# Performance work log

Measured on AMD Instinct MI355X. Metric: run time of the kernel, lower is better.

## Reference

```python
import jax, jax.numpy as jnp
import numpy as np

N_NODES = 100000
N_EDGES = 400000
HIDDEN = 256
N_LAYERS = 4
HEADS = 8
MAX_DEPTH = 20
NUM_GRAPHS = 128
SEQ_LEN = 5
VOCAB = 5002  # vocab_size + 2
NEG_SLOPE = 0.2
BN_EPS = 1e-5


def setup_inputs() -> dict:
    key = jax.random.key(0)
    ks = jax.random.split(key, 16)
    x = jax.random.randint(ks[0], (N_NODES, 2), 0, 98, dtype=jnp.int32)
    node_depth = jax.random.randint(ks[1], (N_NODES, 1), 0, MAX_DEPTH + 1, dtype=jnp.int32)
    edge_index = jax.random.randint(ks[2], (2, N_EDGES), 0, N_NODES, dtype=jnp.int32)
    batch = jnp.sort(jax.random.randint(ks[3], (N_NODES,), 0, NUM_GRAPHS, dtype=jnp.int32))
    s = 1.0 / np.sqrt(HIDDEN)
    return {
        "x": x,
        "node_depth": node_depth,
        "edge_index": edge_index,
        "batch": batch,
        "type_emb": jax.random.normal(ks[4], (98, HIDDEN), jnp.float32) * s,
        "attr_emb": jax.random.normal(ks[5], (10030, HIDDEN), jnp.float32) * s,
        "depth_emb": jax.random.normal(ks[6], (MAX_DEPTH + 1, HIDDEN), jnp.float32) * s,
        "Ws": jax.random.normal(ks[7], (N_LAYERS, HIDDEN, HIDDEN), jnp.float32) * s,
        "att_src": jax.random.normal(ks[8], (N_LAYERS, HIDDEN), jnp.float32) * s,
        "att_dst": jax.random.normal(ks[9], (N_LAYERS, HIDDEN), jnp.float32) * s,
        "gat_bias": jnp.zeros((N_LAYERS, HIDDEN), jnp.float32),
        "bn_gamma": jnp.ones((N_LAYERS, HIDDEN), jnp.float32),
        "bn_beta": jnp.zeros((N_LAYERS, HIDDEN), jnp.float32),
        "tok_W": jax.random.normal(ks[10], (SEQ_LEN, HIDDEN, VOCAB), jnp.float32) * s,
        "tok_b": jnp.zeros((SEQ_LEN, VOCAB), jnp.float32),
    }


def _gat_layer(h, src, dst, W, a_src, a_dst, bias, heads):
    # h: [N, HIDDEN]; PyG GATConv v1 with concat heads, self-loops already in (src, dst)
    N = h.shape[0]
    d = HIDDEN // heads
    hh = (h @ W).reshape(N, heads, d)                       # [N, H, d]
    s_src = jnp.einsum("nhd,hd->nh", hh, a_src.reshape(heads, d))
    s_dst = jnp.einsum("nhd,hd->nh", hh, a_dst.reshape(heads, d))
    e = jax.nn.leaky_relu(s_src[src] + s_dst[dst], NEG_SLOPE)  # [E, H]
    m = jax.ops.segment_max(e, dst, num_segments=N)           # [N, H]
    ex = jnp.exp(e - m[dst])
    denom = jax.ops.segment_sum(ex, dst, num_segments=N)      # [N, H]
    alpha = ex / denom[dst]                                    # [E, H]
    msg = hh[src] * alpha[:, :, None]                          # [E, H, d]
    out = jax.ops.segment_sum(msg, dst, num_segments=N)       # [N, H, d]
    return out.reshape(N, HIDDEN) + bias


def _batchnorm(h, gamma, beta):
    mu = jnp.mean(h, axis=0)
    var = jnp.var(h, axis=0)
    return (h - mu) * jax.lax.rsqrt(var + BN_EPS) * gamma + beta


def reference(x, node_depth, edge_index, batch, type_emb, attr_emb, depth_emb,
              Ws, att_src, att_dst, gat_bias, bn_gamma, bn_beta, tok_W, tok_b):
    N = x.shape[0]
    depth = jnp.minimum(node_depth.reshape(-1), MAX_DEPTH)
    h = type_emb[x[:, 0]] + attr_emb[x[:, 1]] + depth_emb[depth]  # [N, HIDDEN]

    # add self loops (PyG GATConv default)
    loop = jnp.arange(N, dtype=edge_index.dtype)
    src = jnp.concatenate([edge_index[0], loop])
    dst = jnp.concatenate([edge_index[1], loop])

    heads_per_layer = [HEADS] * (N_LAYERS - 1) + [1]
    for l in range(N_LAYERS):
        identity = h
        h = _gat_layer(h, src, dst, Ws[l], att_src[l], att_dst[l], gat_bias[l], heads_per_layer[l])
        h = _batchnorm(h, bn_gamma[l], bn_beta[l])
        h = jax.nn.relu(h)
        h = h + identity  # residual

    # mean pool per graph
    counts = jax.ops.segment_sum(jnp.ones((N,), h.dtype), batch, num_segments=NUM_GRAPHS)
    g = jax.ops.segment_sum(h, batch, num_segments=NUM_GRAPHS) / jnp.maximum(counts, 1.0)[:, None]

    # seq_len token predictors -> [SEQ_LEN, G, VOCAB]
    preds = jnp.einsum("gh,shv->sgv", g, tok_W) + tok_b[:, None, :]
    return preds
```

## Files before the change

kernel.cpp:

```cpp
#include <hip/hip_runtime.h>
#include <stdint.h>

typedef uint16_t u16;
typedef uint32_t u32;

#define N_NODESC 100000
#define N_EDGESC 400000
#define E_TOT    500000
#define HID      256
#define NLAYERS  4
#define NGRAPHS  128
#define SEQLEN   5
#define VOCABC   5002
#define MAXDEPTH 20
#define NEG_SLOPE 0.2f
#define BN_EPSC  1e-5f
#define NCHUNK   ((N_NODESC + 255)/256)
#define NCH64    ((N_NODESC + 63)/64)
#define NROWT    (N_NODESC/16)
#define NPART    64
#define NVQ      ((VOCABC + 63)/64)
#define ATTNB    2048
#define LDSROW   264

typedef __attribute__((ext_vector_type(8))) short short8;
typedef __attribute__((ext_vector_type(4))) float f32x4;
typedef __attribute__((ext_vector_type(4))) unsigned short u16x4;

__device__ __forceinline__ float b2f(u16 u){
  union { u32 i; float f; } v; v.i = ((u32)u) << 16; return v.f;
}
__device__ __forceinline__ u16 f2b(float f){
  union { float f; u32 i; } v; v.f = f;
  u32 u = v.i;
  u += 0x7FFFu + ((u >> 16) & 1u);
  return (u16)(u >> 16);
}
__device__ __forceinline__ float ldp(const void* p, size_t i, int f){
  return f ? ((const float*)p)[i] : b2f(((const u16*)p)[i]);
}
__device__ __forceinline__ f32x4 ld4(const void* p, size_t i, int f){
  f32x4 r;
  if (f){
    r = *(const f32x4*)((const float*)p + i);
  } else {
    const u16x4 u = *(const u16x4*)((const u16*)p + i);
    r[0] = b2f(u[0]); r[1] = b2f(u[1]); r[2] = b2f(u[2]); r[3] = b2f(u[3]);
  }
  return r;
}

__global__ __launch_bounds__(64) void k_detect(const void* temb, int* flag){
  int lane = threadIdx.x;
  const u32* w32 = (const u32*)temb;
  int sf = 0, sb = 0;
  for (int i = lane; i < 256; i += 64){
    u32 w = w32[i];
    union { u32 u; float f; } cf; cf.u = w;
    float af = fabsf(cf.f);
    if (cf.f == 0.0f || (af >= 1e-12f && af <= 4096.f)) sf++;
    float b0 = b2f((u16)(w & 0xFFFFu));
    float b1 = b2f((u16)(w >> 16));
    float a0 = fabsf(b0), a1 = fabsf(b1);
    if (b0 == 0.f || (a0 >= 1e-12f && a0 <= 4096.f)) sb++;
    if (b1 == 0.f || (a1 >= 1e-12f && a1 <= 4096.f)) sb++;
  }
  #pragma unroll
  for (int o = 1; o < 64; o <<= 1){ sf += __shfl_xor(sf, o); sb += __shfl_xor(sb, o); }
  if (lane == 0) *flag = (2*sf > sb) ? 1 : 0;
}

__global__ __launch_bounds__(256) void k_zero(int* __restrict__ p, int n){
  int i = blockIdx.x*256 + threadIdx.x;
  if (i < n) p[i] = 0;
}

__global__ __launch_bounds__(256) void k_embed(const int* __restrict__ x, const int* __restrict__ nd,
    const void* __restrict__ temb, const void* __restrict__ aemb, const void* __restrict__ demb,
    u16* __restrict__ h, const int* __restrict__ flagp, int* __restrict__ cursor){
  int f = *flagp;
  int tid = threadIdx.x;
  int r0 = blockIdx.x*64;
  if (tid < 64 && r0 + tid < N_NODESC) cursor[r0 + tid] = 0;
  int wid = tid >> 6, lane = tid & 63;
  int c4 = lane*4;
  #pragma unroll 4
  for (int k = 0; k < 16; ++k){
    int n = r0 + wid*16 + k;
    if (n >= N_NODESC) break;
    int t = x[n*2+0], a = x[n*2+1];
    if (t < 0) t = 0; if (t > 97) t = 97;
    if (a < 0) a = 0; if (a > 10029) a = 10029;
    int d = nd[n]; if (d > MAXDEPTH) d = MAXDEPTH; if (d < 0) d = 0;
    const f32x4 vt = ld4(temb, (size_t)t*HID + c4, f);
    const f32x4 va = ld4(aemb, (size_t)a*HID + c4, f);
    const f32x4 vd = ld4(demb, (size_t)d*HID + c4, f);
    u16x4 o;
    #pragma unroll
    for (int j = 0; j < 4; ++j) o[j] = f2b(vt[j] + va[j] + vd[j]);
    *(u16x4*)(h + (size_t)n*HID + c4) = o;
  }
}

__global__ __launch_bounds__(256) void k_hist(const int* __restrict__ ei, int* __restrict__ cnt){
  int e = blockIdx.x*256 + threadIdx.x;
  if (e >= E_TOT) return;
  int dst = (e < N_EDGESC) ? ei[N_EDGESC + e] : (e - N_EDGESC);
  if ((unsigned)dst >= N_NODESC) return;
  atomicAdd(&cnt[dst], 1);
}

__global__ __launch_bounds__(256) void k_scan_part(const int* __restrict__ cnt,
    int* __restrict__ off, int* __restrict__ btot){
  __shared__ int lds[256];
  int b = blockIdx.x, tid = threadIdx.x;
  int i = b*256 + tid;
  int v = (i < N_NODESC) ? cnt[i] : 0;
  lds[tid] = v;
  __syncthreads();
  #pragma unroll
  for (int s = 1; s < 256; s <<= 1){
    int t = (tid >= s) ? lds[tid - s] : 0;
    __syncthreads();
    lds[tid] += t;
    __syncthreads();
  }
  if (i < N_NODESC) off[i] = lds[tid] - v;
  if (tid == 255) btot[b] = lds[255];
}

__global__ __launch_bounds__(256) void k_scan_tot(const int* __restrict__ btot,
    int* __restrict__ boff, int* __restrict__ offN){
  __shared__ int lds[256];
  __shared__ int s_carry;
  int tid = threadIdx.x;
  if (tid == 0) s_carry = 0;
  __syncthreads();
  for (int base = 0; base < NCHUNK; base += 256){
    int i = base + tid;
    int v = (i < NCHUNK) ? btot[i] : 0;
    lds[tid] = v;
    __syncthreads();
    #pragma unroll
    for (int s = 1; s < 256; s <<= 1){
      int t = (tid >= s) ? lds[tid - s] : 0;
      __syncthreads();
      lds[tid] += t;
      __syncthreads();
    }
    if (i < NCHUNK) boff[i] = s_carry + lds[tid] - v;
    __syncthreads();
    if (tid == 255) s_carry += lds[255];
    __syncthreads();
  }
  if (tid == 0) *offN = s_carry;
}

__global__ __launch_bounds__(256) void k_scan_add(int* __restrict__ off,
    const int* __restrict__ boff, int* __restrict__ cursor){
  int b = blockIdx.x;
  int i = b*256 + threadIdx.x;
  if (i < N_NODESC){ off[i] += boff[b]; cursor[i] = 0; }
}

__global__ __launch_bounds__(256) void k_scatter(const int* __restrict__ ei,
    const int* __restrict__ soff, int* __restrict__ cursor, int* __restrict__ ssorted){
  int e = blockIdx.x*256 + threadIdx.x;
  if (e >= E_TOT) return;
  int src = (e < N_EDGESC) ? ei[e]            : (e - N_EDGESC);
  int dst = (e < N_EDGESC) ? ei[N_EDGESC + e] : (e - N_EDGESC);
  if ((unsigned)dst >= N_NODESC || (unsigned)src >= N_NODESC) return;
  int pos = soff[dst] + atomicAdd(&cursor[dst], 1);
  if ((unsigned)pos < E_TOT) ssorted[pos] = src;
}

__global__ __launch_bounds__(256) void k_transW(const void* __restrict__ W, u16* __restrict__ WT,
    const int* __restrict__ flagp){
  int f = *flagp;
  int l = blockIdx.y, n2 = blockIdx.x, k = threadIdx.x;
  WT[(l*HID + n2)*HID + k] = f2b(ldp(W, (size_t)(l*HID + k)*HID + n2, f));
}

__global__ __launch_bounds__(256) void k_prepVA(const void* __restrict__ Ws,
    const void* __restrict__ asrc, const void* __restrict__ adst,
    u16* __restrict__ VAT, const int* __restrict__ flagp){
  int f = *flagp;
  int l = blockIdx.x;
  int i = threadIdx.x;
  int H = (l == NLAYERS-1) ? 1 : 8;
  float col[16];
  #pragma unroll
  for (int c = 0; c < 16; ++c) col[c] = 0.f;
  if (H == 8){
    for (int h = 0; h < 8; ++h){
      float vs = 0.f, vd = 0.f;
      for (int o = h*32; o < h*32+32; ++o){
        float w = ldp(Ws, ((size_t)l*HID + i)*HID + o, f);
        vs += w * ldp(asrc, (size_t)l*HID + o, f);
        vd += w * ldp(adst, (size_t)l*HID + o, f);
      }
      col[h*2] = vs; col[h*2+1] = vd;
    }
  } else {
    float vs = 0.f, vd = 0.f;
    for (int o = 0; o < HID; ++o){
      float w = ldp(Ws, ((size_t)l*HID + i)*HID + o, f);
      vs += w * ldp(asrc, (size_t)l*HID + o, f);
      vd += w * ldp(adst, (size_t)l*HID + o, f);
    }
    col[0] = vs; col[1] = vd;
  }
  #pragma unroll
  for (int c = 0; c < 16; ++c)
    VAT[((size_t)l*16 + c)*HID + i] = f2b(col[c]);
}

__global__ __launch_bounds__(256) void k_gemm(u16* __restrict__ h,
    const u16* __restrict__ gout, const float* __restrict__ scale,
    const float* __restrict__ shift, int doApply,
    const u16* __restrict__ WT, const u16* __restrict__ VAT,
    u16* __restrict__ hh, float* __restrict__ ssrc, float* __restrict__ sdst,
    int H, float* __restrict__ bnpart){
  __shared__ u16 hA[2][16*LDSROW];
  int tid = threadIdx.x;
  if (blockIdx.x < NPART*2) bnpart[blockIdx.x*256 + tid] = 0.f;
  int wave = tid >> 6, lane = tid & 63;
  int m = lane & 15, quad = lane >> 4;
  int prow = tid >> 4, pch = (tid & 15)*16;

  short8 B[4][8];
  #pragma unroll
  for (int j = 0; j < 4; ++j){
    const u16* wp = WT + (size_t)((wave*4 + j)*16 + m)*HID + quad*8;
    #pragma unroll
    for (int ks = 0; ks < 8; ++ks)
      B[j][ks] = *(const short8*)(wp + ks*32);
  }
  short8 B5[8];
  if (wave == 0){
    const u16* vp = VAT + (size_t)m*HID + quad*8;
    #pragma unroll
    for (int ks = 0; ks < 8; ++ks)
      B5[ks] = *(const short8*)(vp + ks*32);
  }

  f32x4 sc0 = {}, sc1 = {}, sc2 = {}, sc3 = {};
  f32x4 sh0 = {}, sh1 = {}, sh2 = {}, sh3 = {};
  if (doApply){
    sc0 = *(const f32x4*)(scale + pch);      sh0 = *(const f32x4*)(shift + pch);
    sc1 = *(const f32x4*)(scale + pch + 4);  sh1 = *(const f32x4*)(shift + pch + 4);
    sc2 = *(const f32x4*)(scale + pch + 8);  sh2 = *(const f32x4*)(shift + pch + 8);
    sc3 = *(const f32x4*)(scale + pch + 12); sh3 = *(const f32x4*)(shift + pch + 12);
  }

  int t = blockIdx.x;
  if (t >= NROWT) return;

  short8 h0, h1, g0 = {}, g1 = {};
  {
    size_t base = (size_t)(t*16 + prow)*HID + pch;
    h0 = *(const short8*)(h + base);
    h1 = *(const short8*)(h + base + 8);
    if (doApply){
      g0 = *(const short8*)(gout + base);
      g1 = *(const short8*)(gout + base + 8);
    }
  }

  int p = 0;
  for (;;){
    {
      size_t base = (size_t)(t*16 + prow)*HID + pch;
      if (doApply){
        #pragma unroll
        for (int j = 0; j < 4; ++j){
          float tv = b2f((u16)g0[j])*sc0[j] + sh0[j];
          tv = (tv > 0.f) ? tv : 0.f;
          h0[j] = (short)f2b(b2f((u16)h0[j]) + tv);
        }
        #pragma unroll
        for (int j = 0; j < 4; ++j){
          float tv = b2f((u16)g0[4+j])*sc1[j] + sh1[j];
          tv = (tv > 0.f) ? tv : 0.f;
          h0[4+j] = (short)f2b(b2f((u16)h0[4+j]) + tv);
        }
        #pragma unroll
        for (int j = 0; j < 4; ++j){
          float tv = b2f((u16)g1[j])*sc2[j] + sh2[j];
          tv = (tv > 0.f) ? tv : 0.f;
          h1[j] = (short)f2b(b2f((u16)h1[j]) + tv);
        }
        #pragma unroll
        for (int j = 0; j < 4; ++j){
          float tv = b2f((u16)g1[4+j])*sc3[j] + sh3[j];
          tv = (tv > 0.f) ? tv : 0.f;
          h1[4+j] = (short)f2b(b2f((u16)h1[4+j]) + tv);
        }
        *(short8*)(h + base)     = h0;
        *(short8*)(h + base + 8) = h1;
      }
      *(short8*)(&hA[p][prow*LDSROW + pch])     = h0;
      *(short8*)(&hA[p][prow*LDSROW + pch + 8]) = h1;
    }

    int tn = t + gridDim.x;
    bool hn = (tn < NROWT);
    short8 nh0 = h0, nh1 = h1, ng0 = g0, ng1 = g1;
    if (hn){
      size_t nbase = (size_t)(tn*16 + prow)*HID + pch;
      nh0 = *(const short8*)(h + nbase);
      nh1 = *(const short8*)(h + nbase + 8);
      if (doApply){
        ng0 = *(const short8*)(gout + nbase);
        ng1 = *(const short8*)(gout + nbase + 8);
      }
    }

    asm volatile("s_waitcnt lgkmcnt(0)" ::: "memory");
    __builtin_amdgcn_s_barrier();

    short8 A[8];
    #pragma unroll
    for (int ks = 0; ks < 8; ++ks)
      A[ks] = *(const short8*)(&hA[p][m*LDSROW + ks*32 + quad*8]);

    f32x4 acc[4];
    #pragma unroll
    for (int j = 0; j < 4; ++j) acc[j] = (f32x4){0.f,0.f,0.f,0.f};
    #pragma unroll
    for (int ks = 0; ks < 8; ++ks){
      #pragma unroll
      for (int j = 0; j < 4; ++j)
        acc[j] = __builtin_amdgcn_mfma_f32_16x16x32_bf16(A[ks], B[j][ks], acc[j], 0, 0, 0);
    }

    int r0 = t*16;
    if (wave == 0){
      f32x4 acc5 = (f32x4){0.f,0.f,0.f,0.f};
      #pragma unroll
      for (int ks = 0; ks < 8; ++ks)
        acc5 = __builtin_amdgcn_mfma_f32_16x16x32_bf16(A[ks], B5[ks], acc5, 0, 0, 0);
      int hidx = m >> 1, sd = m & 1;
      #pragma unroll
      for (int r = 0; r < 4; ++r){
        int row = r0 + quad*4 + r;
        float val = acc5[r];
        if (H == 8){
          if (sd == 0) ssrc[row*8 + hidx] = val;
          else         sdst[row*8 + hidx] = val;
        } else {
          if (m == 0)      ssrc[row] = val;
          else if (m == 1) sdst[row] = val;
        }
      }
    }

    #pragma unroll
    for (int j = 0; j < 4; ++j){
      int col = (wave*4 + j)*16 + m;
      #pragma unroll
      for (int r = 0; r < 4; ++r){
        int orow = r0 + quad*4 + r;
        hh[(size_t)orow*HID + col] = f2b(acc[j][r]);
      }
    }

    if (!hn) break;
    t = tn; p ^= 1;
    h0 = nh0; h1 = nh1; g0 = ng0; g1 = ng1;
  }
}

__device__ __forceinline__ void attn_node(int n, int lane, const u16* __restrict__ hh,
    const float* __restrict__ ssrc, const float* __restrict__ sdst,
    const int* __restrict__ soff, const int* __restrict__ ssorted, int H, float r[4]){
  int f0 = lane*4;
  int hl = (H == 8) ? (lane >> 3) : 0;
  float sd = sdst[n*H + hl];
  int beg = soff[n], end = soff[n+1];
  if (beg < 0) beg = 0;
  if (end > E_TOT) end = E_TOT;
  r[0] = r[1] = r[2] = r[3] = 0.f;
  if (beg >= end) return;
  int src = ssorted[beg];
  if ((unsigned)src >= N_NODESC) src = n;
  u16x4 hvv = *(const u16x4*)(hh + (size_t)src*HID + f0);
  float es = ssrc[src*H + hl];
  float lval = 0.f;
  float o0 = 0.f, o1 = 0.f, o2 = 0.f, o3 = 0.f;
  for (int i = beg; i < end; ++i){
    int nsrc = src;
    if (i + 1 < end){
      nsrc = ssorted[i+1];
      if ((unsigned)nsrc >= N_NODESC) nsrc = src;
    }
    const u16x4 nh = *(const u16x4*)(hh + (size_t)nsrc*HID + f0);
    const float nes = ssrc[nsrc*H + hl];
    float ev = es + sd;
    ev = (ev > 0.f) ? ev : NEG_SLOPE*ev;
    ev = fminf(fmaxf(ev, -60.f), 60.f);
    float wv = __expf(ev);
    lval += wv;
    o0 += wv*b2f(hvv[0]);
    o1 += wv*b2f(hvv[1]);
    o2 += wv*b2f(hvv[2]);
    o3 += wv*b2f(hvv[3]);
    hvv = nh; es = nes;
  }
  float inv = (lval > 0.f) ? 1.f/lval : 0.f;
  r[0] = o0*inv; r[1] = o1*inv; r[2] = o2*inv; r[3] = o3*inv;
}

__global__ __launch_bounds__(256) void k_attn_gout(const u16* __restrict__ hh,
    const float* __restrict__ ssrc, const float* __restrict__ sdst,
    const int* __restrict__ soff, const int* __restrict__ ssorted,
    u16* __restrict__ gout, int H, float* __restrict__ bnpart){
  __shared__ float lsum[4*HID];
  __shared__ float lsq[4*HID];
  int wid = threadIdx.x >> 6, lane = threadIdx.x & 63;
  int f0 = lane*4;
  float s[4] = {0.f,0.f,0.f,0.f}, q[4] = {0.f,0.f,0.f,0.f};
  int gw = blockIdx.x*4 + wid;
  int nw = gridDim.x*4;
  for (int n = gw; n < N_NODESC; n += nw){
    float r[4];
    attn_node(n, lane, hh, ssrc, sdst, soff, ssorted, H, r);
    u16x4 o;
    #pragma unroll
    for (int j = 0; j < 4; ++j){
      o[j] = f2b(r[j]);
      s[j] += r[j];
      q[j] += r[j]*r[j];
    }
    *(u16x4*)(gout + (size_t)n*HID + f0) = o;
  }
  #pragma unroll
  for (int j = 0; j < 4; ++j){
    lsum[wid*HID + f0 + j] = s[j];
    lsq [wid*HID + f0 + j] = q[j];
  }
  __syncthreads();
  int c = threadIdx.x;
  float ts = lsum[c] + lsum[HID+c] + lsum[2*HID+c] + lsum[3*HID+c];
  float tq = lsq[c]  + lsq[HID+c]  + lsq[2*HID+c]  + lsq[3*HID+c];
  float* prow = bnpart + (size_t)(blockIdx.x & (NPART-1))*512;
  atomicAdd(&prow[c], ts);
  atomicAdd(&prow[HID + c], tq);
}

__global__ __launch_bounds__(256) void k_attn_stats(const u16* __restrict__ hh,
    const float* __restrict__ ssrc, const float* __restrict__ sdst,
    const int* __restrict__ soff, const int* __restrict__ ssorted,
    float* __restrict__ bnpart, int H){
  __shared__ float lsum[4*HID];
  __shared__ float lsq[4*HID];
  int wid = threadIdx.x >> 6, lane = threadIdx.x & 63;
  int gw = blockIdx.x*4 + wid;
  int nw = gridDim.x*4;
  float s[4] = {0.f,0.f,0.f,0.f}, q[4] = {0.f,0.f,0.f,0.f};
  for (int n = gw; n < N_NODESC; n += nw){
    float r[4];
    attn_node(n, lane, hh, ssrc, sdst, soff, ssorted, H, r);
    #pragma unroll
    for (int j = 0; j < 4; ++j){ s[j] += r[j]; q[j] += r[j]*r[j]; }
  }
  int f0 = lane*4;
  #pragma unroll
  for (int j = 0; j < 4; ++j){ lsum[wid*HID + f0 + j] = s[j]; lsq[wid*HID + f0 + j] = q[j]; }
  __syncthreads();
  int c = threadIdx.x;
  float ts = lsum[c] + lsum[HID+c] + lsum[2*HID+c] + lsum[3*HID+c];
  float tq = lsq[c]  + lsq[HID+c]  + lsq[2*HID+c]  + lsq[3*HID+c];
  float* prow = bnpart + (size_t)(blockIdx.x & (NPART-1))*512;
  atomicAdd(&prow[c], ts);
  atomicAdd(&prow[HID + c], tq);
}

__global__ __launch_bounds__(256) void k_attn_apply(const u16* __restrict__ hh,
    const float* __restrict__ ssrc, const float* __restrict__ sdst,
    const int* __restrict__ soff, const int* __restrict__ ssorted,
    const float* __restrict__ scale, const float* __restrict__ shift,
    u16* __restrict__ h, int H){
  int wid = threadIdx.x >> 6, lane = threadIdx.x & 63;
  int n = blockIdx.x*4 + wid;
  if (n >= N_NODESC) return;
  float r[4];
  attn_node(n, lane, hh, ssrc, sdst, soff, ssorted, H, r);
  int f0 = lane*4;
  const f32x4 sc = *(const f32x4*)(scale + f0);
  const f32x4 sh = *(const f32x4*)(shift + f0);
  u16x4 hv = *(u16x4*)(h + (size_t)n*HID + f0);
  u16x4 o;
  #pragma unroll
  for (int j = 0; j < 4; ++j){
    float t = r[j]*sc[j] + sh[j];
    t = (t > 0.f) ? t : 0.f;
    o[j] = f2b(b2f(hv[j]) + t);
  }
  *(u16x4*)(h + (size_t)n*HID + f0) = o;
}

__global__ __launch_bounds__(256) void k_bn_final(const float* __restrict__ bnpart,
    const void* __restrict__ gamma, const void* __restrict__ beta,
    float* __restrict__ scale, float* __restrict__ shift,
    const int* __restrict__ flagp, int loff){
  int f = *flagp;
  int c = threadIdx.x;
  float s = 0.f, q = 0.f;
  #pragma unroll 4
  for (int p = 0; p < NPART; ++p){
    s += bnpart[(size_t)p*512 + c];
    q += bnpart[(size_t)p*512 + HID + c];
  }
  float mu  = s * (1.f/N_NODESC);
  float var = q * (1.f/N_NODESC) - mu*mu;
  if (!(var >= 0.f)) var = 0.f;
  float sc = ldp(gamma, (size_t)loff + c, f) * rsqrtf(var + BN_EPSC);
  scale[c] = sc;
  shift[c] = ldp(beta, (size_t)loff + c, f) - mu*sc;
}

__global__ __launch_bounds__(256) void k_pool(const u16* __restrict__ h,
    const int* __restrict__ batch, float* __restrict__ gsum, int* __restrict__ gcnt){
  int c = threadIdx.x;
  int r0 = blockIdx.x * 256;
  int r1 = min(r0 + 256, N_NODESC);
  if (r0 >= N_NODESC) return;
  int cur = batch[r0];
  float acc = 0.f;
  int nacc = 0;
  for (int r = r0; r < r1; ++r){
    int b = batch[r];
    if ((unsigned)b >= NGRAPHS) continue;
    if (b != cur){
      if ((unsigned)cur < NGRAPHS){
        atomicAdd(&gsum[cur*HID + c], acc);
        if (c == 0) atomicAdd(&gcnt[cur], nacc);
      }
      acc = 0.f; nacc = 0; cur = b;
    }
    acc += b2f(h[(size_t)r*HID + c]);
    nacc++;
  }
  if ((unsigned)cur < NGRAPHS){
    atomicAdd(&gsum[cur*HID + c], acc);
    if (c == 0) atomicAdd(&gcnt[cur], nacc);
  }
}

__global__ __launch_bounds__(256) void k_pool_fused(const u16* __restrict__ h,
    const u16* __restrict__ gout, const float* __restrict__ scale, const float* __restrict__ shift,
    const int* __restrict__ batch, float* __restrict__ gsum, int* __restrict__ gcnt){
  __shared__ int lb[64];
  int tid = threadIdx.x;
  int r0 = blockIdx.x*64;
  if (tid < 64){
    int rr = r0 + tid;
    lb[tid] = (rr < N_NODESC) ? batch[rr] : -1;
  }
  __syncthreads();
  int wid = tid >> 6, lane = tid & 63;
  int c4 = lane*4;
  const f32x4 sc = *(const f32x4*)(scale + c4);
  const f32x4 sh = *(const f32x4*)(shift + c4);
  int rbase = r0 + wid*16;
  f32x4 acc = (f32x4){0.f,0.f,0.f,0.f};
  int nacc = 0, cur = -1;
  #pragma unroll 4
  for (int k = 0; k < 16; ++k){
    int r = rbase + k;
    if (r >= N_NODESC) break;
    int b = lb[wid*16 + k];
    if ((unsigned)b >= NGRAPHS) continue;
    if (b != cur){
      if ((unsigned)cur < NGRAPHS){
        atomicAdd(&gsum[cur*HID + c4+0], acc[0]);
        atomicAdd(&gsum[cur*HID + c4+1], acc[1]);
        atomicAdd(&gsum[cur*HID + c4+2], acc[2]);
        atomicAdd(&gsum[cur*HID + c4+3], acc[3]);
        if (lane == 0) atomicAdd(&gcnt[cur], nacc);
      }
      acc = (f32x4){0.f,0.f,0.f,0.f}; nacc = 0; cur = b;
    }
    const u16x4 hv = *(const u16x4*)(h    + (size_t)r*HID + c4);
    const u16x4 gv = *(const u16x4*)(gout + (size_t)r*HID + c4);
    #pragma unroll
    for (int j = 0; j < 4; ++j){
      float t = b2f(gv[j])*sc[j] + sh[j];
      t = (t > 0.f) ? t : 0.f;
      acc[j] += b2f(hv[j]) + t;
    }
    nacc++;
  }
  if ((unsigned)cur < NGRAPHS){
    atomicAdd(&gsum[cur*HID + c4+0], acc[0]);
    atomicAdd(&gsum[cur*HID + c4+1], acc[1]);
    atomicAdd(&gsum[cur*HID + c4+2], acc[2]);
    atomicAdd(&gsum[cur*HID + c4+3], acc[3]);
    if (lane == 0) atomicAdd(&gcnt[cur], nacc);
  }
}

__global__ __launch_bounds__(256) void k_gprep(const float* __restrict__ gsum,
    const int* __restrict__ gcnt, u16* __restrict__ gbf){
  int g = blockIdx.x, c = threadIdx.x;
  int cc = gcnt[g]; if (cc < 1) cc = 1;
  gbf[g*HID + c] = f2b(gsum[(size_t)g*HID + c] * (1.f/(float)cc));
}

__global__ __launch_bounds__(256) void k_pred(const u16* __restrict__ gbf,
    const void* __restrict__ tokW, const void* __restrict__ tokb, void* __restrict__ out,
    const int* __restrict__ flagp){
  int f = *flagp;
  int wave = threadIdx.x >> 6, lane = threadIdx.x & 63;
  int m = lane & 15, quad = lane >> 4;
  int s = blockIdx.y;
  int v = blockIdx.x*64 + wave*16 + m;
  bool vok = (v < VOCABC);

  f32x4 acc[8];
  #pragma unroll
  for (int t = 0; t < 8; ++t) acc[t] = (f32x4){0.f,0.f,0.f,0.f};

  const size_t wrow = (size_t)s*HID*VOCABC + v;
  #pragma unroll
  for (int ks = 0; ks < 8; ++ks){
    int kb = ks*32 + quad*8;
    short8 b;
    #pragma unroll
    for (int j = 0; j < 8; ++j)
      b[j] = vok ? (short)f2b(ldp(tokW, wrow + (size_t)(kb + j)*VOCABC, f)) : (short)0;
    #pragma unroll
    for (int t = 0; t < 8; ++t){
      const short8 a = *(const short8*)(gbf + (size_t)(t*16 + m)*HID + kb);
      acc[t] = __builtin_amdgcn_mfma_f32_16x16x32_bf16(a, b, acc[t], 0, 0, 0);
    }
  }

  float bb = vok ? ldp(tokb, (size_t)s*VOCABC + v, f) : 0.f;
  if (!vok) return;
  #pragma unroll
  for (int t = 0; t < 8; ++t){
    #pragma unroll
    for (int r = 0; r < 4; ++r){
      int grow = t*16 + quad*4 + r;
      float val = acc[t][r] + bb;
      size_t oi = ((size_t)(s*NGRAPHS + grow)*VOCABC) + v;
      if (f) ((float*)out)[oi] = val;
      else   ((u16*)out)[oi]   = f2b(val);
    }
  }
}

extern "C" void kernel_launch(void* const* d_in, const int* in_sizes, int n_in,
                              void* d_out, int out_size, void* d_ws, size_t ws_size,
                              hipStream_t stream) {
  const int* x          = (const int*)d_in[0];
  const int* node_depth = (const int*)d_in[1];
  const int* edge_index = (const int*)d_in[2];
  const int* batch      = (const int*)d_in[3];
  const void* type_emb  = d_in[4];
  const void* attr_emb  = d_in[5];
  const void* depth_emb = d_in[6];
  const void* Ws        = d_in[7];
  const void* att_src   = d_in[8];
  const void* att_dst   = d_in[9];
  const void* bn_gamma  = d_in[11];
  const void* bn_beta   = d_in[12];
  const void* tok_W     = d_in[13];
  const void* tok_b     = d_in[14];

  char* base = (char*)d_ws;
  size_t off = 0;
  auto carve = [&](size_t bytes) -> void* {
    void* p = base + off;
    off += (bytes + 255) & ~(size_t)255;
    return p;
  };
  u16*   h     = (u16*)carve((size_t)N_NODESC*HID*2);
  u16*   hh    = (u16*)carve((size_t)N_NODESC*HID*2);
  float* ssrc  = (float*)carve((size_t)N_NODESC*8*4);
  float* sdst  = (float*)carve((size_t)N_NODESC*8*4);
  int*   soff  = (int*)carve((size_t)(N_NODESC+1)*4);
  int*   cursor= (int*)carve((size_t)N_NODESC*4);
  int*   ssorted=(int*)carve((size_t)E_TOT*4);
  int*   btot  = (int*)carve((size_t)NCHUNK*4);
  int*   boff  = (int*)carve((size_t)NCHUNK*4);
  u16*   WT    = (u16*)carve((size_t)NLAYERS*HID*HID*2);
  u16*   VAT   = (u16*)carve((size_t)NLAYERS*16*HID*2);
  float* bnpart= (float*)carve((size_t)NPART*512*4);
  float* bnscale=(float*)carve(HID*4);
  float* bnshift=(float*)carve(HID*4);
  float* gsum  = (float*)carve((size_t)NGRAPHS*HID*4);
  int*   gcnt  = (int*)carve((size_t)NGRAPHS*4);
  u16*   gbf   = (u16*)carve((size_t)NGRAPHS*HID*2);
  int*   dflag = (int*)carve(256);
  size_t common = off;
  u16*   gout  = (u16*)carve((size_t)N_NODESC*HID*2);
  const bool useGout = (off <= ws_size);
  if (common > ws_size) return;

  const int EB  = (E_TOT + 255)/256;
  const int NB4 = (N_NODESC + 3)/4;

  k_detect<<<1, 64, 0, stream>>>(type_emb, dflag);

  k_embed<<<NCH64, 256, 0, stream>>>(x, node_depth, type_emb, attr_emb, depth_emb, h, dflag, cursor);
  k_transW<<<dim3(256, NLAYERS), 256, 0, stream>>>(Ws, WT, dflag);
  k_prepVA<<<NLAYERS, 256, 0, stream>>>(Ws, att_src, att_dst, VAT, dflag);
  k_hist<<<EB, 256, 0, stream>>>(edge_index, cursor);
  k_scan_part<<<NCHUNK, 256, 0, stream>>>(cursor, soff, btot);
  k_scan_tot<<<1, 256, 0, stream>>>(btot, boff, soff + N_NODESC);
  k_scan_add<<<NCHUNK, 256, 0, stream>>>(soff, boff, cursor);
  k_scatter<<<EB, 256, 0, stream>>>(edge_index, soff, cursor, ssorted);

  for (int l = 0; l < NLAYERS; ++l){
    int H = (l == NLAYERS-1) ? 1 : 8;
    int doApply = (useGout && l > 0) ? 1 : 0;
    k_gemm<<<1024, 256, 0, stream>>>(h, gout, bnscale, bnshift, doApply,
                                     WT + (size_t)l*HID*HID, VAT + (size_t)l*16*HID,
                                     hh, ssrc, sdst, H, bnpart);
    if (useGout){
      k_attn_gout<<<ATTNB, 256, 0, stream>>>(hh, ssrc, sdst, soff, ssorted, gout, H, bnpart);
      k_bn_final<<<1, 256, 0, stream>>>(bnpart, bn_gamma, bn_beta, bnscale, bnshift, dflag, l*HID);
    } else {
      k_attn_stats<<<2048, 256, 0, stream>>>(hh, ssrc, sdst, soff, ssorted, bnpart, H);
      k_bn_final<<<1, 256, 0, stream>>>(bnpart, bn_gamma, bn_beta, bnscale, bnshift, dflag, l*HID);
      k_attn_apply<<<NB4, 256, 0, stream>>>(hh, ssrc, sdst, soff, ssorted, bnscale, bnshift, h, H);
    }
  }

  k_zero<<<(NGRAPHS*HID + NGRAPHS + 255)/256, 256, 0, stream>>>((int*)gsum, NGRAPHS*HID + NGRAPHS);
  if (useGout)
    k_pool_fused<<<NCH64, 256, 0, stream>>>(h, gout, bnscale, bnshift, batch, gsum, gcnt);
  else
    k_pool<<<NCHUNK, 256, 0, stream>>>(h, batch, gsum, gcnt);
  k_gprep<<<NGRAPHS, 256, 0, stream>>>(gsum, gcnt, gbf);

  k_pred<<<dim3(NVQ, SEQLEN), 256, 0, stream>>>(gbf, tok_W, tok_b, d_out, dflag);
}
```

Measured before the change: 798.1 us.

## Widen GEMM blocks to 512 threads and swap MFMA operands for vector stores

The node-feature GEMM kernel now runs 8 waves per block, each owning 2 column tiles instead of 4. This halves the B fragments held in registers per wave and splits the row-tile load across more threads. The MFMA operands are swapped so each lane holds 4 consecutive output channels of one node, which turns scattered 2-byte stores of hh into 8-byte vector stores. Per-block work is spread over more waves, at the cost of higher block-level synchronization per tile and a different register/occupancy balance.

```diff
diff --git a/kernel.cpp b/kernel.cpp
--- a/kernel.cpp
+++ b/kernel.cpp
@@ -215,7 +215,7 @@
     VAT[((size_t)l*16 + c)*HID + i] = f2b(col[c]);
 }
 
-__global__ __launch_bounds__(256) void k_gemm(u16* __restrict__ h,
+__global__ __launch_bounds__(512) void k_gemm(u16* __restrict__ h,
     const u16* __restrict__ gout, const float* __restrict__ scale,
     const float* __restrict__ shift, int doApply,
     const u16* __restrict__ WT, const u16* __restrict__ VAT,
@@ -223,18 +223,18 @@
     int H, float* __restrict__ bnpart){
   __shared__ u16 hA[2][16*LDSROW];
   int tid = threadIdx.x;
-  if (blockIdx.x < NPART*2) bnpart[blockIdx.x*256 + tid] = 0.f;
+  if (blockIdx.x < NPART) bnpart[blockIdx.x*512 + tid] = 0.f;
   int wave = tid >> 6, lane = tid & 63;
   int m = lane & 15, quad = lane >> 4;
-  int prow = tid >> 4, pch = (tid & 15)*16;
-
-  short8 B[4][8];
-  #pragma unroll
-  for (int j = 0; j < 4; ++j){
-    const u16* wp = WT + (size_t)((wave*4 + j)*16 + m)*HID + quad*8;
+  int prow = tid >> 5, pch = (tid & 31)*8;
+
+  short8 B[2][8];
+  #pragma unroll
+  for (int jj = 0; jj < 2; ++jj){
+    const u16* wp = WT + (size_t)(((wave*2 + jj)*16 + m)*HID) + quad*8;
     #pragma unroll
     for (int ks = 0; ks < 8; ++ks)
-      B[j][ks] = *(const short8*)(wp + ks*32);
+      B[jj][ks] = *(const short8*)(wp + ks*32);
   }
   short8 B5[8];
   if (wave == 0){
@@ -244,27 +244,20 @@
       B5[ks] = *(const short8*)(vp + ks*32);
   }
 
-  f32x4 sc0 = {}, sc1 = {}, sc2 = {}, sc3 = {};
-  f32x4 sh0 = {}, sh1 = {}, sh2 = {}, sh3 = {};
+  f32x4 sc0 = {}, sc1 = {}, sh0 = {}, sh1 = {};
   if (doApply){
-    sc0 = *(const f32x4*)(scale + pch);      sh0 = *(const f32x4*)(shift + pch);
-    sc1 = *(const f32x4*)(scale + pch + 4);  sh1 = *(const f32x4*)(shift + pch + 4);
-    sc2 = *(const f32x4*)(scale + pch + 8);  sh2 = *(const f32x4*)(shift + pch + 8);
-    sc3 = *(const f32x4*)(scale + pch + 12); sh3 = *(const f32x4*)(shift + pch + 12);
+    sc0 = *(const f32x4*)(scale + pch);     sh0 = *(const f32x4*)(shift + pch);
+    sc1 = *(const f32x4*)(scale + pch + 4); sh1 = *(const f32x4*)(shift + pch + 4);
   }
 
   int t = blockIdx.x;
   if (t >= NROWT) return;
 
-  short8 h0, h1, g0 = {}, g1 = {};
+  short8 h0, g0 = {};
   {
     size_t base = (size_t)(t*16 + prow)*HID + pch;
     h0 = *(const short8*)(h + base);
-    h1 = *(const short8*)(h + base + 8);
-    if (doApply){
-      g0 = *(const short8*)(gout + base);
-      g1 = *(const short8*)(gout + base + 8);
-    }
+    if (doApply) g0 = *(const short8*)(gout + base);
   }
 
   int p = 0;
@@ -284,36 +277,18 @@
           tv = (tv > 0.f) ? tv : 0.f;
           h0[4+j] = (short)f2b(b2f((u16)h0[4+j]) + tv);
         }
-        #pragma unroll
-        for (int j = 0; j < 4; ++j){
-          float tv = b2f((u16)g1[j])*sc2[j] + sh2[j];
-          tv = (tv > 0.f) ? tv : 0.f;
-          h1[j] = (short)f2b(b2f((u16)h1[j]) + tv);
-        }
-        #pragma unroll
-        for (int j = 0; j < 4; ++j){
-          float tv = b2f((u16)g1[4+j])*sc3[j] + sh3[j];
-          tv = (tv > 0.f) ? tv : 0.f;
-          h1[4+j] = (short)f2b(b2f((u16)h1[4+j]) + tv);
-        }
-        *(short8*)(h + base)     = h0;
-        *(short8*)(h + base + 8) = h1;
+        *(short8*)(h + base) = h0;
       }
-      *(short8*)(&hA[p][prow*LDSROW + pch])     = h0;
-      *(short8*)(&hA[p][prow*LDSROW + pch + 8]) = h1;
+      *(short8*)(&hA[p][prow*LDSROW + pch]) = h0;
     }
 
     int tn = t + gridDim.x;
     bool hn = (tn < NROWT);
-    short8 nh0 = h0, nh1 = h1, ng0 = g0, ng1 = g1;
+    short8 nh0 = h0, ng0 = g0;
     if (hn){
       size_t nbase = (size_t)(tn*16 + prow)*HID + pch;
       nh0 = *(const short8*)(h + nbase);
-      nh1 = *(const short8*)(h + nbase + 8);
-      if (doApply){
-        ng0 = *(const short8*)(gout + nbase);
-        ng1 = *(const short8*)(gout + nbase + 8);
-      }
+      if (doApply) ng0 = *(const short8*)(gout + nbase);
     }
 
     asm volatile("s_waitcnt lgkmcnt(0)" ::: "memory");
@@ -324,50 +299,49 @@
     for (int ks = 0; ks < 8; ++ks)
       A[ks] = *(const short8*)(&hA[p][m*LDSROW + ks*32 + quad*8]);
 
-    f32x4 acc[4];
-    #pragma unroll
-    for (int j = 0; j < 4; ++j) acc[j] = (f32x4){0.f,0.f,0.f,0.f};
+    f32x4 acc0 = (f32x4){0.f,0.f,0.f,0.f};
+    f32x4 acc1 = (f32x4){0.f,0.f,0.f,0.f};
     #pragma unroll
     for (int ks = 0; ks < 8; ++ks){
-      #pragma unroll
-      for (int j = 0; j < 4; ++j)
-        acc[j] = __builtin_amdgcn_mfma_f32_16x16x32_bf16(A[ks], B[j][ks], acc[j], 0, 0, 0);
-    }
-
-    int r0 = t*16;
+      acc0 = __builtin_amdgcn_mfma_f32_16x16x32_bf16(B[0][ks], A[ks], acc0, 0, 0, 0);
+      acc1 = __builtin_amdgcn_mfma_f32_16x16x32_bf16(B[1][ks], A[ks], acc1, 0, 0, 0);
+    }
+
+    int node = t*16 + m;
+
     if (wave == 0){
       f32x4 acc5 = (f32x4){0.f,0.f,0.f,0.f};
       #pragma unroll
       for (int ks = 0; ks < 8; ++ks)
-        acc5 = __builtin_amdgcn_mfma_f32_16x16x32_bf16(A[ks], B5[ks], acc5, 0, 0, 0);
-      int hidx = m >> 1, sd = m & 1;
+        acc5 = __builtin_amdgcn_mfma_f32_16x16x32_bf16(B5[ks], A[ks], acc5, 0, 0, 0);
       #pragma unroll
       for (int r = 0; r < 4; ++r){
-        int row = r0 + quad*4 + r;
+        int c = quad*4 + r;
         float val = acc5[r];
         if (H == 8){
-          if (sd == 0) ssrc[row*8 + hidx] = val;
-          else         sdst[row*8 + hidx] = val;
+          int hidx = c >> 1;
+          if ((c & 1) == 0) ssrc[node*8 + hidx] = val;
+          else              sdst[node*8 + hidx] = val;
         } else {
-          if (m == 0)      ssrc[row] = val;
-          else if (m == 1) sdst[row] = val;
+          if (c == 0)      ssrc[node] = val;
+          else if (c == 1) sdst[node] = val;
         }
       }
     }
 
-    #pragma unroll
-    for (int j = 0; j < 4; ++j){
-      int col = (wave*4 + j)*16 + m;
+    {
+      int ch0 = (wave*2 + 0)*16 + quad*4;
+      int ch1 = (wave*2 + 1)*16 + quad*4;
+      u16x4 o0, o1;
       #pragma unroll
-      for (int r = 0; r < 4; ++r){
-        int orow = r0 + quad*4 + r;
-        hh[(size_t)orow*HID + col] = f2b(acc[j][r]);
-      }
+      for (int r = 0; r < 4; ++r){ o0[r] = f2b(acc0[r]); o1[r] = f2b(acc1[r]); }
+      *(u16x4*)(hh + (size_t)node*HID + ch0) = o0;
+      *(u16x4*)(hh + (size_t)node*HID + ch1) = o1;
     }
 
     if (!hn) break;
     t = tn; p ^= 1;
-    h0 = nh0; h1 = nh1; g0 = ng0; g1 = ng1;
+    h0 = nh0; g0 = ng0;
   }
 }
 
@@ -717,7 +691,7 @@
   for (int l = 0; l < NLAYERS; ++l){
     int H = (l == NLAYERS-1) ? 1 : 8;
     int doApply = (useGout && l > 0) ? 1 : 0;
-    k_gemm<<<1024, 256, 0, stream>>>(h, gout, bnscale, bnshift, doApply,
+    k_gemm<<<1024, 512, 0, stream>>>(h, gout, bnscale, bnshift, doApply,
                                      WT + (size_t)l*HID*HID, VAT + (size_t)l*16*HID,
                                      hh, ssrc, sdst, H, bnpart);
     if (useGout){
```

Result: no change. 783.9 us (-1.8%).
